# Kernel optimization log

Hardware: AMD Instinct MI355X
Metric: run time of the kernel (lower is better)

The kernel has to match this reference:

```python
import jax, jax.numpy as jnp
import numpy as np
from jax import lax

B, C_IN, L = 16, 2, 8192
D, H, NL = 256, 8, 4
DK = D // H
DFF = 2 * D
S = L // 8  # downsampled length = 1024
EPS = 1e-5


def _pe(seq, d):
    pos = jnp.arange(seq, dtype=jnp.float32)[:, None]
    div = jnp.exp(jnp.arange(0, d, 2, dtype=jnp.float32) * (-np.log(10000.0) / d))
    pe = jnp.zeros((seq, d), dtype=jnp.float32)
    pe = pe.at[:, 0::2].set(jnp.sin(pos * div))
    pe = pe.at[:, 1::2].set(jnp.cos(pos * div))
    return pe  # (seq, d)


def _layernorm(x, g, b):
    m = jnp.mean(x, axis=-1, keepdims=True)
    v = jnp.mean((x - m) ** 2, axis=-1, keepdims=True)
    return (x - m) * lax.rsqrt(v + EPS) * g + b


def setup_inputs() -> dict:
    key = jax.random.key(0)
    ks = jax.random.split(key, 20)
    sd = 0.02
    inp = {
        'x': jax.random.normal(ks[0], (B, C_IN, L), jnp.float32),
        'conv1_w': jax.random.normal(ks[1], (32, C_IN, 8), jnp.float32) * sd,
        'conv1_b': jnp.zeros((32,), jnp.float32),
        'conv2_w': jax.random.normal(ks[2], (D, 32, 4), jnp.float32) * sd,
        'conv2_b': jnp.zeros((D,), jnp.float32),
        'wq': jax.random.normal(ks[3], (NL, D, D), jnp.float32) * sd,
        'bq': jnp.zeros((NL, D), jnp.float32),
        'wk': jax.random.normal(ks[4], (NL, D, D), jnp.float32) * sd,
        'bk': jnp.zeros((NL, D), jnp.float32),
        'wv': jax.random.normal(ks[5], (NL, D, D), jnp.float32) * sd,
        'bv': jnp.zeros((NL, D), jnp.float32),
        'wo': jax.random.normal(ks[6], (NL, D, D), jnp.float32) * sd,
        'bo': jnp.zeros((NL, D), jnp.float32),
        'ln1_g': jnp.ones((NL, D), jnp.float32),
        'ln1_b': jnp.zeros((NL, D), jnp.float32),
        'ff_w1': jax.random.normal(ks[7], (NL, D, DFF), jnp.float32) * sd,
        'ff_b1': jnp.zeros((NL, DFF), jnp.float32),
        'ff_w2': jax.random.normal(ks[8], (NL, DFF, D), jnp.float32) * sd,
        'ff_b2': jnp.zeros((NL, D), jnp.float32),
        'ln2_g': jnp.ones((NL, D), jnp.float32),
        'ln2_b': jnp.zeros((NL, D), jnp.float32),
        'cls_w1': jax.random.normal(ks[9], (D, D // 2), jnp.float32) * sd,
        'cls_b1': jnp.zeros((D // 2,), jnp.float32),
        'cls_w2': jax.random.normal(ks[10], (D // 2, 1), jnp.float32) * sd,
        'cls_b2': jnp.zeros((1,), jnp.float32),
    }
    return inp


def reference(x, conv1_w, conv1_b, conv2_w, conv2_b,
              wq, bq, wk, bk, wv, bv, wo, bo,
              ln1_g, ln1_b, ff_w1, ff_b1, ff_w2, ff_b2, ln2_g, ln2_b,
              cls_w1, cls_b1, cls_w2, cls_b2):
    dn = ('NCH', 'OIH', 'NCH')
    # downsampler: conv(k8,s4,p2) -> relu -> conv(k4,s2,p1) -> relu
    h = lax.conv_general_dilated(x, conv1_w, (4,), [(2, 2)], dimension_numbers=dn)
    h = jax.nn.relu(h + conv1_b[None, :, None])
    h = lax.conv_general_dilated(h, conv2_w, (2,), [(1, 1)], dimension_numbers=dn)
    h = jax.nn.relu(h + conv2_b[None, :, None])
    h = h.transpose(0, 2, 1)  # (B, S, D)
    h = h + _pe(h.shape[1], D)[None]
    scale = 1.0 / np.sqrt(DK)
    for i in range(NL):
        # multi-head attention (explicit QK^T -> softmax -> V)
        q = (h @ wq[i] + bq[i]).reshape(B, S, H, DK)
        k = (h @ wk[i] + bk[i]).reshape(B, S, H, DK)
        v = (h @ wv[i] + bv[i]).reshape(B, S, H, DK)
        scores = jnp.einsum('bqhd,bkhd->bhqk', q, k) * scale
        attn = jax.nn.softmax(scores, axis=-1)
        ctx = jnp.einsum('bhqk,bkhd->bqhd', attn, v).reshape(B, S, D)
        h = _layernorm(h + ctx @ wo[i] + bo[i], ln1_g[i], ln1_b[i])
        ff = jax.nn.relu(h @ ff_w1[i] + ff_b1[i]) @ ff_w2[i] + ff_b2[i]
        h = _layernorm(h + ff, ln2_g[i], ln2_b[i])
    pooled = jnp.mean(h, axis=1)  # (B, D)
    logits = jax.nn.relu(pooled @ cls_w1 + cls_b1) @ cls_w2 + cls_b2
    return jax.nn.sigmoid(logits)  # (B, 1)
```

## Files before the change

kernel.cpp:

```cpp
#include <hip/hip_runtime.h>
#include <math.h>

typedef unsigned short u16;
typedef __attribute__((ext_vector_type(8))) short bf16x8;
typedef __attribute__((ext_vector_type(4))) float f32x4;
typedef __attribute__((ext_vector_type(16))) float f32x16;

#define B_ 16
#define L_ 8192
#define D_ 256
#define H_ 8
#define NL_ 4
#define DFF_ 512
#define S_ 1024
#define L1_ 2048
#define MROWS_ 16384

__device__ __forceinline__ u16 f2bf(float f) {
    unsigned u = __float_as_uint(f);
    unsigned r = (u + 0x7fffu + ((u >> 16) & 1u)) >> 16;
    return (u16)r;
}
__device__ __forceinline__ float fexp2(float x) {
    return __builtin_amdgcn_exp2f(x);
}
__device__ __forceinline__ unsigned cvtpk(float a, float b) {
    unsigned r;
    asm("v_cvt_pk_bf16_f32 %0, %1, %2" : "=v"(r) : "v"(a), "v"(b));
    return r;
}
__device__ __forceinline__ void pl32swap(unsigned& dst, unsigned& src) {
    asm volatile("v_permlane32_swap_b32 %0, %1" : "+v"(dst), "+v"(src));
}

typedef __attribute__((address_space(1))) const void gvoid;
typedef __attribute__((address_space(3))) void lvoid;
__device__ __forceinline__ void gll16(const void* g, void* l) {
    __builtin_amdgcn_global_load_lds((gvoid*)g, (lvoid*)l, 16, 0, 0);
}
__device__ __forceinline__ void stage64(const u16* src, int ld, u16* lds, int tid) {
    gll16(src + (size_t)(tid >> 2) * ld + (tid & 3) * 8, lds + (tid >> 6) * 512);
}

__global__ __launch_bounds__(256) void conv1_kernel(const float* __restrict__ x,
                                                    const float* __restrict__ w,
                                                    const float* __restrict__ bias,
                                                    float* __restrict__ out) {
    int idx = blockIdx.x * 256 + threadIdx.x;
    int t = idx & 2047;
    int o = (idx >> 11) & 31;
    int b = idx >> 16;
    float s = bias[o];
    int base = t * 4 - 2;
#pragma unroll
    for (int c = 0; c < 2; ++c) {
        const float* xr = x + ((size_t)(b * 2 + c)) * L_;
        const float* wr = w + (o * 2 + c) * 8;
#pragma unroll
        for (int j = 0; j < 8; ++j) {
            int p = base + j;
            if (p >= 0 && p < L_) s += xr[p] * wr[j];
        }
    }
    out[idx] = fmaxf(s, 0.f);
}

__global__ __launch_bounds__(256) void im2col2_kernel(const float* __restrict__ h1,
                                                      u16* __restrict__ A2) {
    int idx = blockIdx.x * 256 + threadIdx.x;
    int k = idx & 127, row = idx >> 7;
    int c = k >> 2, j = k & 3;
    int b = row >> 10, s = row & 1023;
    int p = s * 2 - 1 + j;
    float v = (p >= 0 && p < L1_) ? h1[((size_t)(b * 32 + c) << 11) + p] : 0.f;
    A2[idx] = f2bf(v);
}

__global__ __launch_bounds__(256) void pack_all(const float* __restrict__ wq,
                                                const float* __restrict__ wk,
                                                const float* __restrict__ wv,
                                                const float* __restrict__ wo,
                                                const float* __restrict__ ff_w1,
                                                const float* __restrict__ ff_w2,
                                                const float* __restrict__ conv2_w,
                                                const float* __restrict__ bq,
                                                const float* __restrict__ bk,
                                                const float* __restrict__ bv,
                                                u16* __restrict__ qkvT, u16* __restrict__ woT,
                                                u16* __restrict__ ff1T, u16* __restrict__ ff2T,
                                                u16* __restrict__ w2cT,
                                                float* __restrict__ pe, float* __restrict__ bqkv,
                                                float* __restrict__ pooled, float qscale) {
    int id = blockIdx.x * 256 + threadIdx.x;
    if (id < 786432) {
        int l = id / 196608, j = id % 196608;
        int row = j >> 8, k = j & 255;
        const float* src; float sc = 1.f; int n;
        if (row < 256) { src = wq; n = row; sc = qscale; }
        else if (row < 512) { src = wk; n = row - 256; }
        else { src = wv; n = row - 512; }
        qkvT[id] = f2bf(src[((size_t)l * 256 + k) * 256 + n] * sc);
        return;
    }
    id -= 786432;
    if (id < 262144) {
        int l = id >> 16, j = id & 65535;
        int n = j >> 8, k = j & 255;
        woT[id] = f2bf(wo[((size_t)l * 256 + k) * 256 + n]);
        return;
    }
    id -= 262144;
    if (id < 524288) {
        int l = id >> 17, j = id & 131071;
        int n = j >> 8, k = j & 255;
        ff1T[id] = f2bf(ff_w1[((size_t)l * 256 + k) * 512 + n]);
        return;
    }
    id -= 524288;
    if (id < 524288) {
        int l = id >> 17, j = id & 131071;
        int n = j >> 9, k = j & 511;
        ff2T[id] = f2bf(ff_w2[((size_t)l * 512 + k) * 256 + n]);
        return;
    }
    id -= 524288;
    if (id < 32768) { w2cT[id] = f2bf(conv2_w[id]); return; }
    id -= 32768;
    if (id < 262144) {
        int s = id >> 8, d = id & 255;
        int i2 = d & ~1;
        float div = expf((float)i2 * (-9.210340371976184f / 256.f));
        float arg = (float)s * div;
        pe[id] = (d & 1) ? cosf(arg) : sinf(arg);
        return;
    }
    id -= 262144;
    if (id < 3072) {
        int l = id / 768, n = id % 768;
        const float* src = (n < 256) ? bq : (n < 512) ? bk : bv;
        float sc = (n < 256) ? qscale : 1.f;
        bqkv[id] = src[l * 256 + (n & 255)] * sc;
        return;
    }
    id -= 3072;
    if (id < 4096) pooled[id] = 0.f;
}

template <int EP>
__global__ __launch_bounds__(256) void mfma_gemm128(const u16* __restrict__ A, int lda,
                                                    const u16* __restrict__ WT,
                                                    const float* __restrict__ bias,
                                                    const float* __restrict__ pe,
                                                    float* __restrict__ hout,
                                                    u16* __restrict__ outB,
                                                    u16* __restrict__ ktout,
                                                    u16* __restrict__ vtout,
                                                    int N, int K) {
    __shared__ u16 Alds[128 * 32];
    __shared__ u16 Blds[128 * 32];
    int tid = threadIdx.x;
    int lane = tid & 63, w = tid >> 6;
    int lo = lane & 15, hi = lane >> 4;
    int m0 = blockIdx.y * 128;
    int n0 = blockIdx.x * 128;
    int wm = (w >> 1) * 64, wn = (w & 1) * 64;
    f32x4 acc[4][4];
#pragma unroll
    for (int i = 0; i < 4; ++i)
#pragma unroll
        for (int j = 0; j < 4; ++j) acc[i][j] = (f32x4){0.f, 0.f, 0.f, 0.f};

    for (int k0 = 0; k0 < K; k0 += 32) {
        stage64(A + (size_t)m0 * lda + k0, lda, Alds, tid);
        stage64(A + (size_t)(m0 + 64) * lda + k0, lda, Alds + 2048, tid);
        stage64(WT + (size_t)n0 * K + k0, K, Blds, tid);
        stage64(WT + (size_t)(n0 + 64) * K + k0, K, Blds + 2048, tid);
        __syncthreads();
        bf16x8 af[4], bfr[4];
#pragma unroll
        for (int mf = 0; mf < 4; ++mf) af[mf] = *(bf16x8*)&Alds[(wm + mf * 16 + lo) * 32 + hi * 8];
#pragma unroll
        for (int nf = 0; nf < 4; ++nf) bfr[nf] = *(bf16x8*)&Blds[(wn + nf * 16 + lo) * 32 + hi * 8];
#pragma unroll
        for (int mf = 0; mf < 4; ++mf)
#pragma unroll
            for (int nf = 0; nf < 4; ++nf)
                acc[mf][nf] = __builtin_amdgcn_mfma_f32_16x16x32_bf16(af[mf], bfr[nf], acc[mf][nf], 0, 0, 0);
        __syncthreads();
    }
#pragma unroll
    for (int mf = 0; mf < 4; ++mf)
#pragma unroll
        for (int nf = 0; nf < 4; ++nf) {
            int col = n0 + wn + nf * 16 + lo;
            float bb = bias[col];
            int rowb = m0 + wm + mf * 16 + hi * 4;
            if (EP == 3 && col >= 512) {
                int dc = col - 512;
                int bhh = ((rowb >> 10) << 3) + (dc >> 5);
                int s = rowb & 1023;
                unsigned u0 = (unsigned)f2bf(acc[mf][nf][0] + bb) |
                              ((unsigned)f2bf(acc[mf][nf][1] + bb) << 16);
                unsigned u1 = (unsigned)f2bf(acc[mf][nf][2] + bb) |
                              ((unsigned)f2bf(acc[mf][nf][3] + bb) << 16);
                uint2 val = {u0, u1};
                *(uint2*)(vtout + (((size_t)bhh * 32 + (s >> 5)) * 32 + (dc & 31)) * 32 + (s & 31)) = val;
            } else if (EP == 3 && col >= 256) {
                int kc = col - 256;
                int bhh = ((rowb >> 10) << 3) + (kc >> 5);
                int s = rowb & 1023;
                u16* kt_base = ktout + (((size_t)bhh * 32 + (s >> 5)) * 32) * 32;
#pragma unroll
                for (int r = 0; r < 4; ++r)
                    kt_base[((s & 31) + r) * 32 + (kc & 31)] = f2bf(acc[mf][nf][r] + bb);
            } else {
#pragma unroll
                for (int r = 0; r < 4; ++r) {
                    float v = acc[mf][nf][r] + bb;
                    if (EP == 1 || EP == 2) v = fmaxf(v, 0.f);
                    if (EP == 2) {
                        v += pe[((rowb + r) & 1023) * 256 + col];
                        hout[(size_t)(rowb + r) * 256 + col] = v;
                        outB[(size_t)(rowb + r) * 256 + col] = f2bf(v);
                    } else if (EP == 3) {
                        outB[(size_t)(rowb + r) * 256 + col] = f2bf(v);
                    } else {
                        outB[(size_t)(rowb + r) * N + col] = f2bf(v);
                    }
                }
            }
        }
}

template <int LAST>
__global__ __launch_bounds__(256) void mfma_gemm_ln(const u16* __restrict__ A, int lda,
                                                    const u16* __restrict__ WT,
                                                    const float* __restrict__ bias,
                                                    const float* __restrict__ resid,
                                                    const float* __restrict__ g,
                                                    const float* __restrict__ b2,
                                                    float* __restrict__ hout,
                                                    u16* __restrict__ hbout,
                                                    float* __restrict__ pooled,
                                                    int K) {
    __shared__ u16 Alds[32 * 32];
    __shared__ u16 Blds[256 * 32];
    __shared__ float red1[32][4];
    __shared__ float red2[32][4];
    int tid = threadIdx.x;
    int lane = tid & 63, w = tid >> 6;
    int lo = lane & 15, hi = lane >> 4;
    int m0 = blockIdx.x * 32;
    int wn = w * 64;
    f32x4 acc[2][4];
#pragma unroll
    for (int i = 0; i < 2; ++i)
#pragma unroll
        for (int j = 0; j < 4; ++j) acc[i][j] = (f32x4){0.f, 0.f, 0.f, 0.f};

    for (int k0 = 0; k0 < K; k0 += 32) {
        if (tid < 128)
            gll16(A + (size_t)(m0 + (tid >> 2)) * lda + k0 + (tid & 3) * 8, Alds + (tid >> 6) * 512);
        stage64(WT + (size_t)0 * K + k0, K, Blds, tid);
        stage64(WT + (size_t)64 * K + k0, K, Blds + 2048, tid);
        stage64(WT + (size_t)128 * K + k0, K, Blds + 4096, tid);
        stage64(WT + (size_t)192 * K + k0, K, Blds + 6144, tid);
        __syncthreads();
        bf16x8 af[2], bfr[4];
#pragma unroll
        for (int mf = 0; mf < 2; ++mf) af[mf] = *(bf16x8*)&Alds[(mf * 16 + lo) * 32 + hi * 8];
#pragma unroll
        for (int nf = 0; nf < 4; ++nf) bfr[nf] = *(bf16x8*)&Blds[(wn + nf * 16 + lo) * 32 + hi * 8];
#pragma unroll
        for (int mf = 0; mf < 2; ++mf)
#pragma unroll
            for (int nf = 0; nf < 4; ++nf)
                acc[mf][nf] = __builtin_amdgcn_mfma_f32_16x16x32_bf16(af[mf], bfr[nf], acc[mf][nf], 0, 0, 0);
        __syncthreads();
    }

#pragma unroll
    for (int mf = 0; mf < 2; ++mf)
#pragma unroll
        for (int nf = 0; nf < 4; ++nf) {
            int col = wn + nf * 16 + lo;
            float bb = bias[col];
#pragma unroll
            for (int r = 0; r < 4; ++r) {
                int row = m0 + mf * 16 + hi * 4 + r;
                acc[mf][nf][r] += bb + resid[(size_t)row * 256 + col];
            }
        }
#pragma unroll
    for (int mf = 0; mf < 2; ++mf)
#pragma unroll
        for (int r = 0; r < 4; ++r) {
            float s1 = acc[mf][0][r] + acc[mf][1][r] + acc[mf][2][r] + acc[mf][3][r];
            float s2 = acc[mf][0][r] * acc[mf][0][r] + acc[mf][1][r] * acc[mf][1][r] +
                       acc[mf][2][r] * acc[mf][2][r] + acc[mf][3][r] * acc[mf][3][r];
#pragma unroll
            for (int off = 1; off < 16; off <<= 1) {
                s1 += __shfl_xor(s1, off);
                s2 += __shfl_xor(s2, off);
            }
            if (lo == 0) {
                red1[mf * 16 + hi * 4 + r][w] = s1;
                red2[mf * 16 + hi * 4 + r][w] = s2;
            }
        }
    __syncthreads();
    float colsum[4] = {0.f, 0.f, 0.f, 0.f};
#pragma unroll
    for (int mf = 0; mf < 2; ++mf)
#pragma unroll
        for (int r = 0; r < 4; ++r) {
            int rl = mf * 16 + hi * 4 + r;
            float mean = (red1[rl][0] + red1[rl][1] + red1[rl][2] + red1[rl][3]) * (1.f / 256.f);
            float e2 = (red2[rl][0] + red2[rl][1] + red2[rl][2] + red2[rl][3]) * (1.f / 256.f);
            float rs = rsqrtf(e2 - mean * mean + 1e-5f);
#pragma unroll
            for (int nf = 0; nf < 4; ++nf) {
                int col = wn + nf * 16 + lo;
                float o = (acc[mf][nf][r] - mean) * rs * g[col] + b2[col];
                if (LAST) {
                    colsum[nf] += o;
                } else {
                    hout[(size_t)(m0 + rl) * 256 + col] = o;
                    hbout[(size_t)(m0 + rl) * 256 + col] = f2bf(o);
                }
            }
        }
    if (LAST) {
        int b = m0 >> 10;
#pragma unroll
        for (int nf = 0; nf < 4; ++nf) {
            float cs = colsum[nf];
            cs += __shfl_xor(cs, 16);
            cs += __shfl_xor(cs, 32);
            if (hi == 0) atomicAdd(&pooled[b * 256 + wn + nf * 16 + lo], cs);
        }
    }
}

__global__ __launch_bounds__(256) void attn_mfma(u16* __restrict__ qbuf,
                                                 const u16* __restrict__ ktiles,
                                                 const u16* __restrict__ vtiles) {
    int tid = threadIdx.x;
    int lane = tid & 63, w = tid >> 6;
    int q = lane & 31, h = lane >> 5;
    int phys = blockIdx.x;
    int bid = (phys & 7) * 128 + (phys >> 3);
    int qt = bid & 7, hh = (bid >> 3) & 7, bb = bid >> 6;
    int q0 = qt * 128 + w * 32;
    size_t rowbase = (size_t)bb * S_;

    const u16* qrow = qbuf + (rowbase + q0 + q) * 256 + hh * 32;
    bf16x8 qf0 = *(const bf16x8*)(qrow + h * 8);
    bf16x8 qf1 = *(const bf16x8*)(qrow + 16 + h * 8);

    const u16* kb = ktiles + (size_t)(bb * 8 + hh) * 32768 + q * 32 + h * 8;
    const u16* vb = vtiles + (size_t)(bb * 8 + hh) * 32768 + q * 32 + h * 8;

    f32x16 O = {0.f, 0.f, 0.f, 0.f, 0.f, 0.f, 0.f, 0.f, 0.f, 0.f, 0.f, 0.f, 0.f, 0.f, 0.f, 0.f};
    float l = 0.f;

#define LOADT(d0, d1, d2, d3, t)                         \
    {                                                    \
        const u16* kr = kb + (t) * 1024;                 \
        d0 = *(const bf16x8*)kr;                         \
        d1 = *(const bf16x8*)(kr + 16);                  \
        const u16* vr = vb + (t) * 1024;                 \
        d2 = *(const bf16x8*)vr;                         \
        d3 = *(const bf16x8*)(vr + 16);                  \
    }

#define TILE_BODY(kf0_, kf1_, vf0_, vf1_)                                               \
    {                                                                                   \
        f32x16 S = {0.f, 0.f, 0.f, 0.f, 0.f, 0.f, 0.f, 0.f,                             \
                    0.f, 0.f, 0.f, 0.f, 0.f, 0.f, 0.f, 0.f};                            \
        S = __builtin_amdgcn_mfma_f32_32x32x16_bf16(kf0_, qf0, S, 0, 0, 0);             \
        S = __builtin_amdgcn_mfma_f32_32x32x16_bf16(kf1_, qf1, S, 0, 0, 0);             \
        _Pragma("unroll") for (int i = 0; i < 16; ++i) S[i] = fexp2(S[i]);              \
        float t0 = (S[0] + S[1]) + (S[2] + S[3]);                                       \
        float t1 = (S[4] + S[5]) + (S[6] + S[7]);                                       \
        float t2 = (S[8] + S[9]) + (S[10] + S[11]);                                     \
        float t3 = (S[12] + S[13]) + (S[14] + S[15]);                                   \
        float ls = (t0 + t1) + (t2 + t3);                                               \
        unsigned ua = __float_as_uint(ls), ub = ua;                                     \
        pl32swap(ua, ub);                                                               \
        l += __uint_as_float(ua) + __uint_as_float(ub);                                 \
        unsigned pk[8];                                                                 \
        _Pragma("unroll") for (int i = 0; i < 8; ++i) pk[i] = cvtpk(S[2 * i], S[2 * i + 1]); \
        pl32swap(pk[2], pk[0]);                                                         \
        pl32swap(pk[3], pk[1]);                                                         \
        pl32swap(pk[6], pk[4]);                                                         \
        pl32swap(pk[7], pk[5]);                                                         \
        uint4 t4 = {pk[0], pk[1], pk[2], pk[3]};                                        \
        uint4 t5 = {pk[4], pk[5], pk[6], pk[7]};                                        \
        bf16x8 pf0 = *(bf16x8*)&t4;                                                     \
        bf16x8 pf1 = *(bf16x8*)&t5;                                                     \
        O = __builtin_amdgcn_mfma_f32_32x32x16_bf16(vf0_, pf0, O, 0, 0, 0);             \
        O = __builtin_amdgcn_mfma_f32_32x32x16_bf16(vf1_, pf1, O, 0, 0, 0);             \
    }

    bf16x8 ka0, ka1, va0, va1, kb0, kb1, vb0, vb1;
    LOADT(ka0, ka1, va0, va1, 0);
    LOADT(kb0, kb1, vb0, vb1, 1);
    for (int kt = 0; kt < 32; kt += 2) {
        bf16x8 kc0 = ka0, kc1 = ka1, vc0 = va0, vc1 = va1;
        if (kt + 2 < 32) LOADT(kc0, kc1, vc0, vc1, kt + 2);
        TILE_BODY(ka0, ka1, va0, va1);
        bf16x8 kd0 = kb0, kd1 = kb1, vd0 = vb0, vd1 = vb1;
        if (kt + 3 < 32) LOADT(kd0, kd1, vd0, vd1, kt + 3);
        TILE_BODY(kb0, kb1, vb0, vb1);
        ka0 = kc0; ka1 = kc1; va0 = vc0; va1 = vc1;
        kb0 = kd0; kb1 = kd1; vb0 = vd0; vb1 = vd1;
    }
#undef LOADT
#undef TILE_BODY

    float inv = 1.f / l;
    u16* orow = qbuf + (rowbase + q0 + q) * 256 + hh * 32;
#pragma unroll
    for (int gg = 0; gg < 4; ++gg) {
        unsigned u0 = cvtpk(O[4 * gg] * inv, O[4 * gg + 1] * inv);
        unsigned u1 = cvtpk(O[4 * gg + 2] * inv, O[4 * gg + 3] * inv);
        uint2 val = {u0, u1};
        *(uint2*)(orow + gg * 8 + h * 4) = val;
    }
}

__global__ __launch_bounds__(256) void cls_kernel(const float* __restrict__ pooled,
                                                  const float* __restrict__ w1,
                                                  const float* __restrict__ b1,
                                                  const float* __restrict__ w2,
                                                  const float* __restrict__ b2,
                                                  float* __restrict__ out) {
    int b = blockIdx.x;
    int d = threadIdx.x;
    __shared__ float pl[256];
    __shared__ float hid[128];
    pl[d] = pooled[b * 256 + d] * (1.f / 1024.f);
    __syncthreads();
    if (d < 128) {
        float a = b1[d];
        for (int k = 0; k < 256; ++k) a += pl[k] * w1[k * 128 + d];
        hid[d] = fmaxf(a, 0.f);
    }
    __syncthreads();
    if (d == 0) {
        float a = b2[0];
        for (int k = 0; k < 128; ++k) a += hid[k] * w2[k];
        out[b] = 1.f / (1.f + expf(-a));
    }
}

extern "C" void kernel_launch(void* const* d_in, const int* in_sizes, int n_in,
                              void* d_out, int out_size, void* d_ws, size_t ws_size,
                              hipStream_t stream) {
    const float* x       = (const float*)d_in[0];
    const float* conv1_w = (const float*)d_in[1];
    const float* conv1_b = (const float*)d_in[2];
    const float* conv2_w = (const float*)d_in[3];
    const float* conv2_b = (const float*)d_in[4];
    const float* wq      = (const float*)d_in[5];
    const float* bq      = (const float*)d_in[6];
    const float* wk      = (const float*)d_in[7];
    const float* bk      = (const float*)d_in[8];
    const float* wv      = (const float*)d_in[9];
    const float* bv      = (const float*)d_in[10];
    const float* wo      = (const float*)d_in[11];
    const float* bo      = (const float*)d_in[12];
    const float* ln1_g   = (const float*)d_in[13];
    const float* ln1_b   = (const float*)d_in[14];
    const float* ff_w1   = (const float*)d_in[15];
    const float* ff_b1   = (const float*)d_in[16];
    const float* ff_w2   = (const float*)d_in[17];
    const float* ff_b2   = (const float*)d_in[18];
    const float* ln2_g   = (const float*)d_in[19];
    const float* ln2_b   = (const float*)d_in[20];
    const float* cls_w1  = (const float*)d_in[21];
    const float* cls_b1  = (const float*)d_in[22];
    const float* cls_w2  = (const float*)d_in[23];
    const float* cls_b2  = (const float*)d_in[24];

    char* wsb = (char*)d_ws;
    float* h    = (float*)wsb;
    u16*   hb   = (u16*)(wsb + ((size_t)16 << 20));
    u16*   qbuf = (u16*)(wsb + ((size_t)24 << 20));
    u16*   ktl  = (u16*)(wsb + ((size_t)32 << 20));
    u16*   vtl  = (u16*)(wsb + ((size_t)40 << 20));
    u16*   ffh  = (u16*)(wsb + ((size_t)32 << 20));
    u16*   A2   = (u16*)(wsb + ((size_t)32 << 20));
    float* h1   = (float*)(wsb + ((size_t)36 << 20));
    float* pe   = (float*)(wsb + ((size_t)48 << 20));
    char*  pkb  = wsb + ((size_t)49 << 20);
    u16*   qkvT = (u16*)pkb;
    u16*   woT  = qkvT + (size_t)4 * 768 * 256;
    u16*   ff1T = woT + (size_t)4 * 256 * 256;
    u16*   ff2T = ff1T + (size_t)4 * 512 * 256;
    u16*   w2cT = ff2T + (size_t)4 * 512 * 256;
    float* bqkv = (float*)(w2cT + 256 * 128);
    float* pooled = bqkv + 4 * 768;

    const float qscale = 0.17677669529663687f * 1.4426950408889634f;
    pack_all<<<9372, 256, 0, stream>>>(wq, wk, wv, wo, ff_w1, ff_w2, conv2_w, bq, bk, bv,
                                       qkvT, woT, ff1T, ff2T, w2cT, pe, bqkv, pooled, qscale);

    conv1_kernel<<<4096, 256, 0, stream>>>(x, conv1_w, conv1_b, h1);
    im2col2_kernel<<<8192, 256, 0, stream>>>(h1, A2);
    mfma_gemm128<2><<<dim3(2, 128), 256, 0, stream>>>(A2, 128, w2cT, conv2_b, pe, h, hb,
                                                      nullptr, nullptr, 256, 128);

    for (int l = 0; l < NL_; ++l) {
        const u16* qkvT_l = qkvT + (size_t)l * 768 * 256;
        const u16* woT_l  = woT + (size_t)l * 256 * 256;
        const u16* ff1T_l = ff1T + (size_t)l * 512 * 256;
        const u16* ff2T_l = ff2T + (size_t)l * 256 * 512;

        mfma_gemm128<3><<<dim3(6, 128), 256, 0, stream>>>(hb, 256, qkvT_l, bqkv + l * 768,
                                                          nullptr, nullptr, qbuf, ktl, vtl, 256, 256);
        attn_mfma<<<1024, 256, 0, stream>>>(qbuf, ktl, vtl);
        mfma_gemm_ln<0><<<512, 256, 0, stream>>>(qbuf, 256, woT_l, bo + l * 256, h,
                                                 ln1_g + l * 256, ln1_b + l * 256, h, hb, nullptr, 256);
        mfma_gemm128<1><<<dim3(4, 128), 256, 0, stream>>>(hb, 256, ff1T_l, ff_b1 + l * 512,
                                                          nullptr, nullptr, ffh, nullptr, nullptr, 512, 256);
        if (l < NL_ - 1) {
            mfma_gemm_ln<0><<<512, 256, 0, stream>>>(ffh, 512, ff2T_l, ff_b2 + l * 256, h,
                                                     ln2_g + l * 256, ln2_b + l * 256, h, hb, nullptr, 512);
        } else {
            mfma_gemm_ln<1><<<512, 256, 0, stream>>>(ffh, 512, ff2T_l, ff_b2 + l * 256, h,
                                                     ln2_g + l * 256, ln2_b + l * 256, h, hb, pooled, 512);
        }
    }

    cls_kernel<<<B_, 256, 0, stream>>>(pooled, cls_w1, cls_b1, cls_w2, cls_b2, (float*)d_out);
}
```

Before: 564.9 us.

## Fuse FFN GEMMs into one LDS-resident kernel, fuse conv1 into im2col, add MFMA priority

Fuses conv1 into the im2col kernel, so the conv1 output is recomputed per im2col element instead of being written to and read back from global memory. Replaces the separate FF1 GEMM and the FF2+LayerNorm GEMM with one fused_ff kernel. That kernel keeps the 32x512 ReLU hidden tile in swizzled LDS, which removes the global ffh round trip and one launch per layer. The fused kernel reads A and weights straight from global memory without LDS staging, and conv1 work is duplicated about twofold. It also adds s_setprio around the MFMA blocks in attention.

Result: slower. 598.6 us (+6.0%).

```diff
diff --git a/kernel.cpp b/kernel.cpp
--- a/kernel.cpp
+++ b/kernel.cpp
@@ -32,6 +32,7 @@
 __device__ __forceinline__ void pl32swap(unsigned& dst, unsigned& src) {
     asm volatile("v_permlane32_swap_b32 %0, %1" : "+v"(dst), "+v"(src));
 }
+__device__ __forceinline__ int swz16(int b) { return b ^ ((b >> 3) & 0x18); }
 
 typedef __attribute__((address_space(1))) const void gvoid;
 typedef __attribute__((address_space(3))) void lvoid;
@@ -42,37 +43,31 @@
     gll16(src + (size_t)(tid >> 2) * ld + (tid & 3) * 8, lds + (tid >> 6) * 512);
 }
 
-__global__ __launch_bounds__(256) void conv1_kernel(const float* __restrict__ x,
-                                                    const float* __restrict__ w,
-                                                    const float* __restrict__ bias,
-                                                    float* __restrict__ out) {
-    int idx = blockIdx.x * 256 + threadIdx.x;
-    int t = idx & 2047;
-    int o = (idx >> 11) & 31;
-    int b = idx >> 16;
-    float s = bias[o];
-    int base = t * 4 - 2;
-#pragma unroll
-    for (int c = 0; c < 2; ++c) {
-        const float* xr = x + ((size_t)(b * 2 + c)) * L_;
-        const float* wr = w + (o * 2 + c) * 8;
-#pragma unroll
-        for (int j = 0; j < 8; ++j) {
-            int p = base + j;
-            if (p >= 0 && p < L_) s += xr[p] * wr[j];
-        }
-    }
-    out[idx] = fmaxf(s, 0.f);
-}
-
-__global__ __launch_bounds__(256) void im2col2_kernel(const float* __restrict__ h1,
-                                                      u16* __restrict__ A2) {
+__global__ __launch_bounds__(256) void conv1_im2col_kernel(const float* __restrict__ x,
+                                                           const float* __restrict__ w,
+                                                           const float* __restrict__ bias,
+                                                           u16* __restrict__ A2) {
     int idx = blockIdx.x * 256 + threadIdx.x;
     int k = idx & 127, row = idx >> 7;
     int c = k >> 2, j = k & 3;
     int b = row >> 10, s = row & 1023;
     int p = s * 2 - 1 + j;
-    float v = (p >= 0 && p < L1_) ? h1[((size_t)(b * 32 + c) << 11) + p] : 0.f;
+    float v = 0.f;
+    if (p >= 0 && p < L1_) {
+        float acc = bias[c];
+        int base = p * 4 - 2;
+#pragma unroll
+        for (int ci = 0; ci < 2; ++ci) {
+            const float* xr = x + ((size_t)(b * 2 + ci)) * L_;
+            const float* wr = w + (c * 2 + ci) * 8;
+#pragma unroll
+            for (int jj = 0; jj < 8; ++jj) {
+                int pos = base + jj;
+                if (pos >= 0 && pos < L_) acc += xr[pos] * wr[jj];
+            }
+        }
+        v = fmaxf(acc, 0.f);
+    }
     A2[idx] = f2bf(v);
 }
 
@@ -217,22 +212,19 @@
 #pragma unroll
                 for (int r = 0; r < 4; ++r) {
                     float v = acc[mf][nf][r] + bb;
-                    if (EP == 1 || EP == 2) v = fmaxf(v, 0.f);
+                    if (EP == 2) v = fmaxf(v, 0.f);
                     if (EP == 2) {
                         v += pe[((rowb + r) & 1023) * 256 + col];
                         hout[(size_t)(rowb + r) * 256 + col] = v;
                         outB[(size_t)(rowb + r) * 256 + col] = f2bf(v);
-                    } else if (EP == 3) {
+                    } else {
                         outB[(size_t)(rowb + r) * 256 + col] = f2bf(v);
-                    } else {
-                        outB[(size_t)(rowb + r) * N + col] = f2bf(v);
                     }
                 }
             }
         }
 }
 
-template <int LAST>
 __global__ __launch_bounds__(256) void mfma_gemm_ln(const u16* __restrict__ A, int lda,
                                                     const u16* __restrict__ WT,
                                                     const float* __restrict__ bias,
@@ -241,7 +233,6 @@
                                                     const float* __restrict__ b2,
                                                     float* __restrict__ hout,
                                                     u16* __restrict__ hbout,
-                                                    float* __restrict__ pooled,
                                                     int K) {
     __shared__ u16 Alds[32 * 32];
     __shared__ u16 Blds[256 * 32];
@@ -309,7 +300,6 @@
             }
         }
     __syncthreads();
-    float colsum[4] = {0.f, 0.f, 0.f, 0.f};
 #pragma unroll
     for (int mf = 0; mf < 2; ++mf)
 #pragma unroll
@@ -322,6 +312,135 @@
             for (int nf = 0; nf < 4; ++nf) {
                 int col = wn + nf * 16 + lo;
                 float o = (acc[mf][nf][r] - mean) * rs * g[col] + b2[col];
+                hout[(size_t)(m0 + rl) * 256 + col] = o;
+                hbout[(size_t)(m0 + rl) * 256 + col] = f2bf(o);
+            }
+        }
+}
+
+template <int LAST>
+__global__ __launch_bounds__(256) void fused_ff(const u16* __restrict__ A,
+                                                const u16* __restrict__ W1T,
+                                                const float* __restrict__ b1,
+                                                const u16* __restrict__ W2T,
+                                                const float* __restrict__ b2,
+                                                const float* __restrict__ resid,
+                                                const float* __restrict__ g,
+                                                const float* __restrict__ bln,
+                                                float* __restrict__ hout,
+                                                u16* __restrict__ hbout,
+                                                float* __restrict__ pooled) {
+    __shared__ char hid[16 * 2048];
+    __shared__ float red1[32][4];
+    __shared__ float red2[32][4];
+    int tid = threadIdx.x;
+    int lane = tid & 63, w = tid >> 6;
+    int lo = lane & 15, hi = lane >> 4;
+    int m0 = blockIdx.x * 32;
+
+    {
+        int wn = w * 128;
+        f32x4 acc[2][8];
+#pragma unroll
+        for (int i = 0; i < 2; ++i)
+#pragma unroll
+            for (int j = 0; j < 8; ++j) acc[i][j] = (f32x4){0.f, 0.f, 0.f, 0.f};
+        for (int k0 = 0; k0 < 256; k0 += 32) {
+            bf16x8 af[2], bfr[8];
+#pragma unroll
+            for (int mf = 0; mf < 2; ++mf)
+                af[mf] = *(const bf16x8*)(A + (size_t)(m0 + mf * 16 + lo) * 256 + k0 + hi * 8);
+#pragma unroll
+            for (int nf = 0; nf < 8; ++nf)
+                bfr[nf] = *(const bf16x8*)(W1T + (size_t)(wn + nf * 16 + lo) * 256 + k0 + hi * 8);
+#pragma unroll
+            for (int mf = 0; mf < 2; ++mf)
+#pragma unroll
+                for (int nf = 0; nf < 8; ++nf)
+                    acc[mf][nf] = __builtin_amdgcn_mfma_f32_16x16x32_bf16(af[mf], bfr[nf], acc[mf][nf], 0, 0, 0);
+        }
+#pragma unroll
+        for (int mf = 0; mf < 2; ++mf)
+#pragma unroll
+            for (int nf = 0; nf < 8; ++nf) {
+                int col = wn + nf * 16 + lo;
+                float bb = b1[col];
+                char* tile = hid + (col >> 5) * 2048;
+                int c2 = (col & 31) * 2;
+#pragma unroll
+                for (int r = 0; r < 4; ++r) {
+                    int row = mf * 16 + hi * 4 + r;
+                    *(u16*)(tile + swz16(row * 64 + c2)) = f2bf(fmaxf(acc[mf][nf][r] + bb, 0.f));
+                }
+            }
+    }
+    __syncthreads();
+
+    int wn = w * 64;
+    f32x4 acc[2][4];
+#pragma unroll
+    for (int i = 0; i < 2; ++i)
+#pragma unroll
+        for (int j = 0; j < 4; ++j) acc[i][j] = (f32x4){0.f, 0.f, 0.f, 0.f};
+    for (int k0 = 0; k0 < 512; k0 += 32) {
+        bf16x8 af[2], bfr[4];
+        const char* tile = hid + (k0 >> 5) * 2048;
+#pragma unroll
+        for (int mf = 0; mf < 2; ++mf)
+            af[mf] = *(const bf16x8*)(tile + swz16((mf * 16 + lo) * 64 + hi * 16));
+#pragma unroll
+        for (int nf = 0; nf < 4; ++nf)
+            bfr[nf] = *(const bf16x8*)(W2T + (size_t)(wn + nf * 16 + lo) * 512 + k0 + hi * 8);
+#pragma unroll
+        for (int mf = 0; mf < 2; ++mf)
+#pragma unroll
+            for (int nf = 0; nf < 4; ++nf)
+                acc[mf][nf] = __builtin_amdgcn_mfma_f32_16x16x32_bf16(af[mf], bfr[nf], acc[mf][nf], 0, 0, 0);
+    }
+
+#pragma unroll
+    for (int mf = 0; mf < 2; ++mf)
+#pragma unroll
+        for (int nf = 0; nf < 4; ++nf) {
+            int col = wn + nf * 16 + lo;
+            float bb = b2[col];
+#pragma unroll
+            for (int r = 0; r < 4; ++r) {
+                int row = m0 + mf * 16 + hi * 4 + r;
+                acc[mf][nf][r] += bb + resid[(size_t)row * 256 + col];
+            }
+        }
+#pragma unroll
+    for (int mf = 0; mf < 2; ++mf)
+#pragma unroll
+        for (int r = 0; r < 4; ++r) {
+            float s1 = acc[mf][0][r] + acc[mf][1][r] + acc[mf][2][r] + acc[mf][3][r];
+            float s2 = acc[mf][0][r] * acc[mf][0][r] + acc[mf][1][r] * acc[mf][1][r] +
+                       acc[mf][2][r] * acc[mf][2][r] + acc[mf][3][r] * acc[mf][3][r];
+#pragma unroll
+            for (int off = 1; off < 16; off <<= 1) {
+                s1 += __shfl_xor(s1, off);
+                s2 += __shfl_xor(s2, off);
+            }
+            if (lo == 0) {
+                red1[mf * 16 + hi * 4 + r][w] = s1;
+                red2[mf * 16 + hi * 4 + r][w] = s2;
+            }
+        }
+    __syncthreads();
+    float colsum[4] = {0.f, 0.f, 0.f, 0.f};
+#pragma unroll
+    for (int mf = 0; mf < 2; ++mf)
+#pragma unroll
+        for (int r = 0; r < 4; ++r) {
+            int rl = mf * 16 + hi * 4 + r;
+            float mean = (red1[rl][0] + red1[rl][1] + red1[rl][2] + red1[rl][3]) * (1.f / 256.f);
+            float e2 = (red2[rl][0] + red2[rl][1] + red2[rl][2] + red2[rl][3]) * (1.f / 256.f);
+            float rs = rsqrtf(e2 - mean * mean + 1e-5f);
+#pragma unroll
+            for (int nf = 0; nf < 4; ++nf) {
+                int col = wn + nf * 16 + lo;
+                float o = (acc[mf][nf][r] - mean) * rs * g[col] + bln[col];
                 if (LAST) {
                     colsum[nf] += o;
                 } else {
@@ -378,8 +497,10 @@
     {                                                                                   \
         f32x16 S = {0.f, 0.f, 0.f, 0.f, 0.f, 0.f, 0.f, 0.f,                             \
                     0.f, 0.f, 0.f, 0.f, 0.f, 0.f, 0.f, 0.f};                            \
+        __builtin_amdgcn_s_setprio(1);                                                  \
         S = __builtin_amdgcn_mfma_f32_32x32x16_bf16(kf0_, qf0, S, 0, 0, 0);             \
         S = __builtin_amdgcn_mfma_f32_32x32x16_bf16(kf1_, qf1, S, 0, 0, 0);             \
+        __builtin_amdgcn_s_setprio(0);                                                  \
         _Pragma("unroll") for (int i = 0; i < 16; ++i) S[i] = fexp2(S[i]);              \
         float t0 = (S[0] + S[1]) + (S[2] + S[3]);                                       \
         float t1 = (S[4] + S[5]) + (S[6] + S[7]);                                       \
@@ -399,8 +520,10 @@
         uint4 t5 = {pk[4], pk[5], pk[6], pk[7]};                                        \
         bf16x8 pf0 = *(bf16x8*)&t4;                                                     \
         bf16x8 pf1 = *(bf16x8*)&t5;                                                     \
+        __builtin_amdgcn_s_setprio(1);                                                  \
         O = __builtin_amdgcn_mfma_f32_32x32x16_bf16(vf0_, pf0, O, 0, 0, 0);             \
         O = __builtin_amdgcn_mfma_f32_32x32x16_bf16(vf1_, pf1, O, 0, 0, 0);             \
+        __builtin_amdgcn_s_setprio(0);                                                  \
     }
 
     bf16x8 ka0, ka1, va0, va1, kb0, kb1, vb0, vb1;
@@ -490,9 +613,7 @@
     u16*   qbuf = (u16*)(wsb + ((size_t)24 << 20));
     u16*   ktl  = (u16*)(wsb + ((size_t)32 << 20));
     u16*   vtl  = (u16*)(wsb + ((size_t)40 << 20));
-    u16*   ffh  = (u16*)(wsb + ((size_t)32 << 20));
     u16*   A2   = (u16*)(wsb + ((size_t)32 << 20));
-    float* h1   = (float*)(wsb + ((size_t)36 << 20));
     float* pe   = (float*)(wsb + ((size_t)48 << 20));
     char*  pkb  = wsb + ((size_t)49 << 20);
     u16*   qkvT = (u16*)pkb;
@@ -507,8 +628,7 @@
     pack_all<<<9372, 256, 0, stream>>>(wq, wk, wv, wo, ff_w1, ff_w2, conv2_w, bq, bk, bv,
                                        qkvT, woT, ff1T, ff2T, w2cT, pe, bqkv, pooled, qscale);
 
-    conv1_kernel<<<4096, 256, 0, stream>>>(x, conv1_w, conv1_b, h1);
-    im2col2_kernel<<<8192, 256, 0, stream>>>(h1, A2);
+    conv1_im2col_kernel<<<8192, 256, 0, stream>>>(x, conv1_w, conv1_b, A2);
     mfma_gemm128<2><<<dim3(2, 128), 256, 0, stream>>>(A2, 128, w2cT, conv2_b, pe, h, hb,
                                                       nullptr, nullptr, 256, 128);
 
@@ -521,16 +641,16 @@
         mfma_gemm128<3><<<dim3(6, 128), 256, 0, stream>>>(hb, 256, qkvT_l, bqkv + l * 768,
                                                           nullptr, nullptr, qbuf, ktl, vtl, 256, 256);
         attn_mfma<<<1024, 256, 0, stream>>>(qbuf, ktl, vtl);
-        mfma_gemm_ln<0><<<512, 256, 0, stream>>>(qbuf, 256, woT_l, bo + l * 256, h,
-                                                 ln1_g + l * 256, ln1_b + l * 256, h, hb, nullptr, 256);
-        mfma_gemm128<1><<<dim3(4, 128), 256, 0, stream>>>(hb, 256, ff1T_l, ff_b1 + l * 512,
-                                                          nullptr, nullptr, ffh, nullptr, nullptr, 512, 256);
+        mfma_gemm_ln<<<512, 256, 0, stream>>>(qbuf, 256, woT_l, bo + l * 256, h,
+                                              ln1_g + l * 256, ln1_b + l * 256, h, hb, 256);
         if (l < NL_ - 1) {
-            mfma_gemm_ln<0><<<512, 256, 0, stream>>>(ffh, 512, ff2T_l, ff_b2 + l * 256, h,
-                                                     ln2_g + l * 256, ln2_b + l * 256, h, hb, nullptr, 512);
+            fused_ff<0><<<512, 256, 0, stream>>>(hb, ff1T_l, ff_b1 + l * 512, ff2T_l,
+                                                 ff_b2 + l * 256, h, ln2_g + l * 256,
+                                                 ln2_b + l * 256, h, hb, nullptr);
         } else {
-            mfma_gemm_ln<1><<<512, 256, 0, stream>>>(ffh, 512, ff2T_l, ff_b2 + l * 256, h,
-                                                     ln2_g + l * 256, ln2_b + l * 256, h, hb, pooled, 512);
+            fused_ff<1><<<512, 256, 0, stream>>>(hb, ff1T_l, ff_b1 + l * 512, ff2T_l,
+                                                 ff_b2 + l * 256, h, ln2_g + l * 256,
+                                                 ln2_b + l * 256, h, hb, pooled);
         }
     }
 
```

## Fuse conv1 into im2col, remap GEMM blocks per XCD, add MFMA priority hints

Applied to the files above, without the earlier changes.

Conv1 is folded into the im2col kernel, so each A2 element recomputes its conv1 output directly from x. This drops the h1 intermediate buffer and one launch, at the cost of redundant conv1 arithmetic (each h1 value is recomputed roughly twice because of overlapping windows). The GEMM and GEMM+LN kernels now use a 1D grid remapped so that consecutive M tiles land on the same XCD (phys&7), aiming for better L2 locality. The attention kernel also wraps its MFMA pairs in s_setprio raises.

Result: faster. 552.7 us (-2.2%).

```diff
diff --git a/kernel.cpp b/kernel.cpp
--- a/kernel.cpp
+++ b/kernel.cpp
@@ -42,37 +42,31 @@
     gll16(src + (size_t)(tid >> 2) * ld + (tid & 3) * 8, lds + (tid >> 6) * 512);
 }
 
-__global__ __launch_bounds__(256) void conv1_kernel(const float* __restrict__ x,
-                                                    const float* __restrict__ w,
-                                                    const float* __restrict__ bias,
-                                                    float* __restrict__ out) {
-    int idx = blockIdx.x * 256 + threadIdx.x;
-    int t = idx & 2047;
-    int o = (idx >> 11) & 31;
-    int b = idx >> 16;
-    float s = bias[o];
-    int base = t * 4 - 2;
-#pragma unroll
-    for (int c = 0; c < 2; ++c) {
-        const float* xr = x + ((size_t)(b * 2 + c)) * L_;
-        const float* wr = w + (o * 2 + c) * 8;
-#pragma unroll
-        for (int j = 0; j < 8; ++j) {
-            int p = base + j;
-            if (p >= 0 && p < L_) s += xr[p] * wr[j];
-        }
-    }
-    out[idx] = fmaxf(s, 0.f);
-}
-
-__global__ __launch_bounds__(256) void im2col2_kernel(const float* __restrict__ h1,
-                                                      u16* __restrict__ A2) {
+__global__ __launch_bounds__(256) void conv1_im2col_kernel(const float* __restrict__ x,
+                                                           const float* __restrict__ w,
+                                                           const float* __restrict__ bias,
+                                                           u16* __restrict__ A2) {
     int idx = blockIdx.x * 256 + threadIdx.x;
     int k = idx & 127, row = idx >> 7;
     int c = k >> 2, j = k & 3;
     int b = row >> 10, s = row & 1023;
     int p = s * 2 - 1 + j;
-    float v = (p >= 0 && p < L1_) ? h1[((size_t)(b * 32 + c) << 11) + p] : 0.f;
+    float v = 0.f;
+    if (p >= 0 && p < L1_) {
+        float acc = bias[c];
+        int base = p * 4 - 2;
+#pragma unroll
+        for (int ci = 0; ci < 2; ++ci) {
+            const float* xr = x + ((size_t)(b * 2 + ci)) * L_;
+            const float* wr = w + (c * 2 + ci) * 8;
+#pragma unroll
+            for (int jj = 0; jj < 8; ++jj) {
+                int pos = base + jj;
+                if (pos >= 0 && pos < L_) acc += xr[pos] * wr[jj];
+            }
+        }
+        v = fmaxf(acc, 0.f);
+    }
     A2[idx] = f2bf(v);
 }
 
@@ -146,7 +140,7 @@
     if (id < 4096) pooled[id] = 0.f;
 }
 
-template <int EP>
+template <int EP, int NT>
 __global__ __launch_bounds__(256) void mfma_gemm128(const u16* __restrict__ A, int lda,
                                                     const u16* __restrict__ WT,
                                                     const float* __restrict__ bias,
@@ -161,8 +155,10 @@
     int tid = threadIdx.x;
     int lane = tid & 63, w = tid >> 6;
     int lo = lane & 15, hi = lane >> 4;
-    int m0 = blockIdx.y * 128;
-    int n0 = blockIdx.x * 128;
+    int phys = blockIdx.x;
+    int cid = phys & 7, idx = phys >> 3;
+    int m0 = (cid * 16 + idx / NT) * 128;
+    int n0 = (idx % NT) * 128;
     int wm = (w >> 1) * 64, wn = (w & 1) * 64;
     f32x4 acc[4][4];
 #pragma unroll
@@ -250,7 +246,8 @@
     int tid = threadIdx.x;
     int lane = tid & 63, w = tid >> 6;
     int lo = lane & 15, hi = lane >> 4;
-    int m0 = blockIdx.x * 32;
+    int phys = blockIdx.x;
+    int m0 = ((phys & 7) * 64 + (phys >> 3)) * 32;
     int wn = w * 64;
     f32x4 acc[2][4];
 #pragma unroll
@@ -378,8 +375,10 @@
     {                                                                                   \
         f32x16 S = {0.f, 0.f, 0.f, 0.f, 0.f, 0.f, 0.f, 0.f,                             \
                     0.f, 0.f, 0.f, 0.f, 0.f, 0.f, 0.f, 0.f};                            \
+        __builtin_amdgcn_s_setprio(1);                                                  \
         S = __builtin_amdgcn_mfma_f32_32x32x16_bf16(kf0_, qf0, S, 0, 0, 0);             \
         S = __builtin_amdgcn_mfma_f32_32x32x16_bf16(kf1_, qf1, S, 0, 0, 0);             \
+        __builtin_amdgcn_s_setprio(0);                                                  \
         _Pragma("unroll") for (int i = 0; i < 16; ++i) S[i] = fexp2(S[i]);              \
         float t0 = (S[0] + S[1]) + (S[2] + S[3]);                                       \
         float t1 = (S[4] + S[5]) + (S[6] + S[7]);                                       \
@@ -399,8 +398,10 @@
         uint4 t5 = {pk[4], pk[5], pk[6], pk[7]};                                        \
         bf16x8 pf0 = *(bf16x8*)&t4;                                                     \
         bf16x8 pf1 = *(bf16x8*)&t5;                                                     \
+        __builtin_amdgcn_s_setprio(1);                                                  \
         O = __builtin_amdgcn_mfma_f32_32x32x16_bf16(vf0_, pf0, O, 0, 0, 0);             \
         O = __builtin_amdgcn_mfma_f32_32x32x16_bf16(vf1_, pf1, O, 0, 0, 0);             \
+        __builtin_amdgcn_s_setprio(0);                                                  \
     }
 
     bf16x8 ka0, ka1, va0, va1, kb0, kb1, vb0, vb1;
@@ -492,7 +493,6 @@
     u16*   vtl  = (u16*)(wsb + ((size_t)40 << 20));
     u16*   ffh  = (u16*)(wsb + ((size_t)32 << 20));
     u16*   A2   = (u16*)(wsb + ((size_t)32 << 20));
-    float* h1   = (float*)(wsb + ((size_t)36 << 20));
     float* pe   = (float*)(wsb + ((size_t)48 << 20));
     char*  pkb  = wsb + ((size_t)49 << 20);
     u16*   qkvT = (u16*)pkb;
@@ -507,10 +507,9 @@
     pack_all<<<9372, 256, 0, stream>>>(wq, wk, wv, wo, ff_w1, ff_w2, conv2_w, bq, bk, bv,
                                        qkvT, woT, ff1T, ff2T, w2cT, pe, bqkv, pooled, qscale);
 
-    conv1_kernel<<<4096, 256, 0, stream>>>(x, conv1_w, conv1_b, h1);
-    im2col2_kernel<<<8192, 256, 0, stream>>>(h1, A2);
-    mfma_gemm128<2><<<dim3(2, 128), 256, 0, stream>>>(A2, 128, w2cT, conv2_b, pe, h, hb,
-                                                      nullptr, nullptr, 256, 128);
+    conv1_im2col_kernel<<<8192, 256, 0, stream>>>(x, conv1_w, conv1_b, A2);
+    mfma_gemm128<2, 2><<<256, 256, 0, stream>>>(A2, 128, w2cT, conv2_b, pe, h, hb,
+                                                nullptr, nullptr, 256, 128);
 
     for (int l = 0; l < NL_; ++l) {
         const u16* qkvT_l = qkvT + (size_t)l * 768 * 256;
@@ -518,13 +517,13 @@
         const u16* ff1T_l = ff1T + (size_t)l * 512 * 256;
         const u16* ff2T_l = ff2T + (size_t)l * 256 * 512;
 
-        mfma_gemm128<3><<<dim3(6, 128), 256, 0, stream>>>(hb, 256, qkvT_l, bqkv + l * 768,
-                                                          nullptr, nullptr, qbuf, ktl, vtl, 256, 256);
+        mfma_gemm128<3, 6><<<768, 256, 0, stream>>>(hb, 256, qkvT_l, bqkv + l * 768,
+                                                    nullptr, nullptr, qbuf, ktl, vtl, 256, 256);
         attn_mfma<<<1024, 256, 0, stream>>>(qbuf, ktl, vtl);
         mfma_gemm_ln<0><<<512, 256, 0, stream>>>(qbuf, 256, woT_l, bo + l * 256, h,
                                                  ln1_g + l * 256, ln1_b + l * 256, h, hb, nullptr, 256);
-        mfma_gemm128<1><<<dim3(4, 128), 256, 0, stream>>>(hb, 256, ff1T_l, ff_b1 + l * 512,
-                                                          nullptr, nullptr, ffh, nullptr, nullptr, 512, 256);
+        mfma_gemm128<1, 4><<<512, 256, 0, stream>>>(hb, 256, ff1T_l, ff_b1 + l * 512,
+                                                    nullptr, nullptr, ffh, nullptr, nullptr, 512, 256);
         if (l < NL_ - 1) {
             mfma_gemm_ln<0><<<512, 256, 0, stream>>>(ffh, 512, ff2T_l, ff_b2 + l * 256, h,
                                                      ln2_g + l * 256, ln2_b + l * 256, h, hb, nullptr, 512);
```
